# Kernel tuning notes

Hardware: AMD Instinct MI355X
Metric: run time of the kernel (lower is better)

Reference implementation:

```python
import jax, jax.numpy as jnp
import numpy as np

BN_EPS = 1e-5


def gcn_conv(x, src, dst, n, W, b):
    # PyG GCNConv: h = x @ W; add self-loops; symmetric deg^{-1/2} norm; scatter-add; + bias
    h = x @ W
    sl = jnp.arange(n, dtype=src.dtype)
    src_f = jnp.concatenate([src, sl])
    dst_f = jnp.concatenate([dst, sl])
    deg = jax.ops.segment_sum(jnp.ones_like(dst_f, dtype=h.dtype), dst_f, num_segments=n)
    dis = jnp.where(deg > 0, jax.lax.rsqrt(jnp.maximum(deg, 1.0)), 0.0)
    norm = dis[src_f] * dis[dst_f]                       # [E+N]
    msg = h[src_f] * norm[:, None]                       # gather + scale
    out = jax.ops.segment_sum(msg, dst_f, num_segments=n)  # scatter-add
    return out + b


def batchnorm(x, g, b):
    # training-mode BatchNorm1d (batch statistics), deterministic
    mu = jnp.mean(x, axis=0)
    var = jnp.mean((x - mu) ** 2, axis=0)
    return g * (x - mu) * jax.lax.rsqrt(var + BN_EPS) + b


def setup_inputs() -> dict:
    key = jax.random.key(0)
    ks = jax.random.split(key, 12)
    N, E, F_IN, D, M, G = 40000, 640000, 128, 128, 256, 2000
    x = jax.random.normal(ks[0], (N, F_IN), dtype=jnp.float32)
    edge_index = jax.random.randint(ks[1], (2, E), 0, N, dtype=jnp.int64)
    batch = jnp.sort(jax.random.randint(ks[2], (N,), 0, G, dtype=jnp.int64))
    s = lambda fi: 1.0 / np.sqrt(fi)
    W1 = jax.random.normal(ks[3], (F_IN, D), dtype=jnp.float32) * s(F_IN)
    b1 = jnp.zeros((D,), jnp.float32)
    W2 = jax.random.normal(ks[4], (D, D), dtype=jnp.float32) * s(D)
    b2 = jnp.zeros((D,), jnp.float32)
    bn1_g = jnp.ones((D,), jnp.float32); bn1_b = jnp.zeros((D,), jnp.float32)
    bn2_g = jnp.ones((D,), jnp.float32); bn2_b = jnp.zeros((D,), jnp.float32)
    fc1_w = jax.random.normal(ks[5], (D, M), dtype=jnp.float32) * s(D)
    fc1_b = jnp.zeros((M,), jnp.float32)
    fc2_w = jax.random.normal(ks[6], (M, M), dtype=jnp.float32) * s(M)
    fc2_b = jnp.zeros((M,), jnp.float32)
    fc3_w = jax.random.normal(ks[7], (M, 1), dtype=jnp.float32) * s(M)
    fc3_b = jnp.zeros((1,), jnp.float32)
    return dict(x=x, edge_index=edge_index, batch=batch, num_graphs=G,
                W1=W1, b1=b1, W2=W2, b2=b2,
                bn1_g=bn1_g, bn1_b=bn1_b, bn2_g=bn2_g, bn2_b=bn2_b,
                fc1_w=fc1_w, fc1_b=fc1_b, fc2_w=fc2_w, fc2_b=fc2_b,
                fc3_w=fc3_w, fc3_b=fc3_b)


def reference(x, edge_index, batch, num_graphs, W1, b1, W2, b2,
              bn1_g, bn1_b, bn2_g, bn2_b,
              fc1_w, fc1_b, fc2_w, fc2_b, fc3_w, fc3_b):
    n = x.shape[0]
    src, dst = edge_index[0], edge_index[1]
    h = gcn_conv(x, src, dst, n, W1, b1)
    h = jax.nn.relu(batchnorm(h, bn1_g, bn1_b))
    h = gcn_conv(h, src, dst, n, W2, b2)
    h = jax.nn.relu(batchnorm(h, bn2_g, bn2_b))
    g = jax.ops.segment_sum(h, batch, num_segments=num_graphs)  # scatter_sum pooling [G, D]
    g = jax.nn.relu(g @ fc1_w + fc1_b)   # dropout is identity in eval
    g = jax.nn.relu(g @ fc2_w + fc2_b)
    return g @ fc3_w + fc3_b             # [G, 1]
```

## Files before the change

### kernel.cpp

```cpp
#include <hip/hip_runtime.h>
#include <hip/hip_fp16.h>

#define NN 40000
#define NE 640000
#define DF 128
#define NG 2000
#define NCH 157
#define FILLB 625
#define G1_BLKS 313
#define G2_BLKS 625

typedef unsigned int u32;
typedef __attribute__((ext_vector_type(8))) short short8;
typedef __attribute__((ext_vector_type(4))) float floatx4;

__device__ inline float2 bf2_to_f2(u32 u) {
    return make_float2(__uint_as_float(u << 16), __uint_as_float(u & 0xffff0000u));
}
__device__ inline u32 f_to_bf(float f) {
    u32 u = __float_as_uint(f);
    return (u + 0x7fffu + ((u >> 16) & 1u)) >> 16;
}
__device__ inline u32 pack_bf2(float a, float b) {
    return f_to_bf(a) | (f_to_bf(b) << 16);
}
__device__ inline float bf_to_f(short s) {
    return __uint_as_float(((u32)(unsigned short)s) << 16);
}
__device__ inline float colw_to_f(int cw) {
    return __half2float(__ushort_as_half((unsigned short)((u32)cw >> 16)));
}

template<bool BF16IN, bool FUSE_BN, bool WT_F32, bool TILE128>
__device__ __forceinline__ void gemm_core(const void* __restrict__ Xv, const void* __restrict__ wsrc,
                                          u32* __restrict__ outb, const float* __restrict__ slots,
                                          const float* __restrict__ gam, const float* __restrict__ bet, int bid) {
    __shared__ unsigned short uni[128 * 136];
    __shared__ float sc[128], sh[128];
    unsigned short* wlds = uni;
    unsigned short* clds = uni;
    int tid = threadIdx.x;
    int row0 = bid * (TILE128 ? 128 : 64);

    if (FUSE_BN) {
        if (tid < 128) {
            float s = 0.f, q = 0.f;
            for (int k = 0; k < 64; k++) {
                s += slots[k * 256 + tid];
                q += slots[k * 256 + 128 + tid];
            }
            const float inv_n = 1.0f / (float)NN;
            float mu = s * inv_n;
            float va = fmaf(-mu, mu, q * inv_n);
            float a = gam[tid] * rsqrtf(va + 1e-5f);
            sc[tid] = a;
            sh[tid] = fmaf(-mu, a, bet[tid]);
        }
    }
    if (WT_F32) {
        const float* W = (const float*)wsrc;
        for (int i = tid; i < 16384; i += 256) {
            int k = i >> 7, c = i & 127;
            wlds[c * 136 + k] = (unsigned short)f_to_bf(W[i]);
        }
    } else {
        const unsigned short* wt = (const unsigned short*)wsrc;
        for (int i = tid; i < 2048; i += 256) {
            int c = i >> 4, s = i & 15;
            *(uint4*)&wlds[c * 136 + s * 8] = ((const uint4*)wt)[i];
        }
    }
    __syncthreads();

    int lane = tid & 63;
    int wave = tid >> 6;
    int qr = lane >> 4;
    int rl = lane & 15;

    if (TILE128) {
        int rA0 = row0 + wave * 32 + rl;
        int rA1 = rA0 + 16;
        int rA0c = rA0 < NN ? rA0 : NN - 1;
        int rA1c = rA1 < NN ? rA1 : NN - 1;
        floatx4 acc[2][8];
#pragma unroll
        for (int a = 0; a < 2; a++)
#pragma unroll
            for (int b = 0; b < 8; b++) acc[a][b] = (floatx4){0.f, 0.f, 0.f, 0.f};
#pragma unroll
        for (int kb = 0; kb < 4; kb++) {
            int k0 = kb * 32 + qr * 8;
            short8 a0, a1;
            if (!BF16IN) {
                const float* p0 = (const float*)Xv + (size_t)rA0c * DF + k0;
                const float* p1 = (const float*)Xv + (size_t)rA1c * DF + k0;
                float4 u0 = *(const float4*)p0, u1 = *(const float4*)(p0 + 4);
                float4 v0 = *(const float4*)p1, v1 = *(const float4*)(p1 + 4);
                float fa[8] = {u0.x, u0.y, u0.z, u0.w, u1.x, u1.y, u1.z, u1.w};
                float fb[8] = {v0.x, v0.y, v0.z, v0.w, v1.x, v1.y, v1.z, v1.w};
#pragma unroll
                for (int j = 0; j < 8; j++) { a0[j] = (short)f_to_bf(fa[j]); a1[j] = (short)f_to_bf(fb[j]); }
            } else {
                a0 = *(const short8*)((const u32*)Xv + (size_t)rA0c * 64 + (k0 >> 1));
                a1 = *(const short8*)((const u32*)Xv + (size_t)rA1c * 64 + (k0 >> 1));
                if (FUSE_BN) {
#pragma unroll
                    for (int j = 0; j < 8; j++) {
                        float f0 = fmaxf(fmaf(bf_to_f(a0[j]), sc[k0 + j], sh[k0 + j]), 0.f);
                        float f1 = fmaxf(fmaf(bf_to_f(a1[j]), sc[k0 + j], sh[k0 + j]), 0.f);
                        a0[j] = (short)f_to_bf(f0);
                        a1[j] = (short)f_to_bf(f1);
                    }
                }
            }
#pragma unroll
            for (int ct = 0; ct < 8; ct++) {
                short8 bfr = *(const short8*)&wlds[(ct * 16 + rl) * 136 + k0];
                acc[0][ct] = __builtin_amdgcn_mfma_f32_16x16x32_bf16(a0, bfr, acc[0][ct], 0, 0, 0);
                acc[1][ct] = __builtin_amdgcn_mfma_f32_16x16x32_bf16(a1, bfr, acc[1][ct], 0, 0, 0);
            }
        }
        __syncthreads();
#pragma unroll
        for (int rt = 0; rt < 2; rt++)
#pragma unroll
            for (int ct = 0; ct < 8; ct++)
#pragma unroll
                for (int r = 0; r < 4; r++) {
                    int lr = wave * 32 + rt * 16 + qr * 4 + r;
                    int c = ct * 16 + rl;
                    clds[lr * 136 + c] = (unsigned short)f_to_bf(acc[rt][ct][r]);
                }
        __syncthreads();
        for (int i = tid; i < 2048; i += 256) {
            int lr = i >> 4, s = i & 15;
            int grow = row0 + lr;
            if (grow < NN) {
                uint4 v = *(const uint4*)&clds[lr * 136 + s * 8];
                ((uint4*)(outb + (size_t)grow * 64))[s] = v;
            }
        }
    } else {
        int rA = row0 + wave * 16 + rl;
        floatx4 acc[8];
#pragma unroll
        for (int b = 0; b < 8; b++) acc[b] = (floatx4){0.f, 0.f, 0.f, 0.f};
#pragma unroll
        for (int kb = 0; kb < 4; kb++) {
            int k0 = kb * 32 + qr * 8;
            short8 a0;
            if (!BF16IN) {
                const float* p0 = (const float*)Xv + (size_t)rA * DF + k0;
                float4 u0 = *(const float4*)p0, u1 = *(const float4*)(p0 + 4);
                float fa[8] = {u0.x, u0.y, u0.z, u0.w, u1.x, u1.y, u1.z, u1.w};
#pragma unroll
                for (int j = 0; j < 8; j++) a0[j] = (short)f_to_bf(fa[j]);
            } else {
                a0 = *(const short8*)((const u32*)Xv + (size_t)rA * 64 + (k0 >> 1));
                if (FUSE_BN) {
#pragma unroll
                    for (int j = 0; j < 8; j++) {
                        float f0 = fmaxf(fmaf(bf_to_f(a0[j]), sc[k0 + j], sh[k0 + j]), 0.f);
                        a0[j] = (short)f_to_bf(f0);
                    }
                }
            }
#pragma unroll
            for (int ct = 0; ct < 8; ct++) {
                short8 bfr = *(const short8*)&wlds[(ct * 16 + rl) * 136 + k0];
                acc[ct] = __builtin_amdgcn_mfma_f32_16x16x32_bf16(a0, bfr, acc[ct], 0, 0, 0);
            }
        }
        __syncthreads();
#pragma unroll
        for (int ct = 0; ct < 8; ct++)
#pragma unroll
            for (int r = 0; r < 4; r++) {
                int lr = wave * 16 + qr * 4 + r;
                int c = ct * 16 + rl;
                clds[lr * 136 + c] = (unsigned short)f_to_bf(acc[ct][r]);
            }
        __syncthreads();
        for (int i = tid; i < 1024; i += 256) {
            int lr = i >> 4, s = i & 15;
            uint4 v = *(const uint4*)&clds[lr * 136 + s * 8];
            ((uint4*)(outb + (size_t)(row0 + lr) * 64))[s] = v;
        }
    }
}

__global__ __launch_bounds__(256, 4) void k_countgemm(const int* __restrict__ dst, int* __restrict__ deg,
                                                      int* __restrict__ rank,
                                                      const float* __restrict__ W1, const float* __restrict__ W2,
                                                      unsigned short* __restrict__ wt2,
                                                      const float* __restrict__ X, u32* __restrict__ outb) {
    int bid = blockIdx.x;
    if (bid < FILLB) {
        int e0 = bid * 1024 + threadIdx.x;
        int d0 = dst[e0], d1 = dst[e0 + 256], d2 = dst[e0 + 512], d3 = dst[e0 + 768];
        int r0 = atomicAdd(&deg[d0], 1);
        int r1 = atomicAdd(&deg[d1], 1);
        int r2 = atomicAdd(&deg[d2], 1);
        int r3 = atomicAdd(&deg[d3], 1);
        rank[e0] = r0;
        rank[e0 + 256] = r1;
        rank[e0 + 512] = r2;
        rank[e0 + 768] = r3;
        return;
    }
    if (bid == FILLB) {
        for (int i = threadIdx.x; i < 128 * 128; i += 256) {
            int k = i >> 7, c = i & 127;
            wt2[c * 128 + k] = (unsigned short)f_to_bf(W2[i]);
        }
        return;
    }
    gemm_core<false, false, true, true>(X, W1, outb, nullptr, nullptr, nullptr, bid - FILLB - 1);
}

__global__ __launch_bounds__(256) void k_scan(const int* __restrict__ deg,
                                              int* __restrict__ row_ptr, float* __restrict__ dis) {
    __shared__ int red[256];
    __shared__ int ls[256];
    int tid = threadIdx.x;
    int blk = blockIdx.x;
    int limit = blk * 256;
    int partial = 0;
    for (int i = tid; i < limit; i += 256) partial += deg[i];
    red[tid] = partial;
    int i = limit + tid;
    int d = (i < NN) ? deg[i] : 0;
    ls[tid] = d;
    __syncthreads();
#pragma unroll
    for (int off = 128; off > 0; off >>= 1) {
        if (tid < off) red[tid] += red[tid + off];
        __syncthreads();
    }
    int base = red[0];
#pragma unroll
    for (int off = 1; off < 256; off <<= 1) {
        int t = (tid >= off) ? ls[tid - off] : 0;
        __syncthreads();
        ls[tid] += t;
        __syncthreads();
    }
    if (i < NN) {
        int r = base + ls[tid] - d;
        row_ptr[i] = r;
        dis[i] = rsqrtf((float)(d + 1));
    }
    if (blk == NCH - 1 && tid == 0) row_ptr[NN] = NE;
}

__global__ __launch_bounds__(256) void k_fill(const int* __restrict__ src, const int* __restrict__ dst,
                                              const int* __restrict__ rank, const int* __restrict__ row_ptr,
                                              const float* __restrict__ dis, u32* __restrict__ col) {
    int e0 = blockIdx.x * 1024 + threadIdx.x;
    int d0 = dst[e0], d1 = dst[e0 + 256], d2 = dst[e0 + 512], d3 = dst[e0 + 768];
    int s0 = src[e0], s1 = src[e0 + 256], s2 = src[e0 + 512], s3 = src[e0 + 768];
    int r0 = rank[e0], r1 = rank[e0 + 256], r2 = rank[e0 + 512], r3 = rank[e0 + 768];
    u32 h0 = (u32)__half_as_ushort(__float2half(dis[s0]));
    u32 h1 = (u32)__half_as_ushort(__float2half(dis[s1]));
    u32 h2 = (u32)__half_as_ushort(__float2half(dis[s2]));
    u32 h3 = (u32)__half_as_ushort(__float2half(dis[s3]));
    col[row_ptr[d0] + r0] = (u32)s0 | (h0 << 16);
    col[row_ptr[d1] + r1] = (u32)s1 | (h1 << 16);
    col[row_ptr[d2] + r2] = (u32)s2 | (h2 << 16);
    col[row_ptr[d3] + r3] = (u32)s3 | (h3 << 16);
}

__global__ __launch_bounds__(256, 4) void k_gemm2(const u32* __restrict__ Hb, const unsigned short* __restrict__ wt2,
                                                  u32* __restrict__ outb, const float* __restrict__ slots,
                                                  const float* __restrict__ gam, const float* __restrict__ bet) {
    gemm_core<true, true, false, false>(Hb, wt2, outb, slots, gam, bet, blockIdx.x);
}

__global__ __launch_bounds__(256) void k_gather(const u32* __restrict__ Hb, const int* __restrict__ row_ptr,
                                                const u32* __restrict__ col, const float* __restrict__ dis,
                                                const float* __restrict__ bias, u32* __restrict__ outb,
                                                float* __restrict__ slots) {
    __shared__ float sred[4][128];
    __shared__ float qred[4][128];
    int t = threadIdx.x & 63;
    int wv = threadIdx.x >> 6;
    int node = blockIdx.x * 4 + wv;
    float di = dis[node];
    float2 acc;
    {
        float2 a = bf2_to_f2(Hb[(size_t)node * 64 + t]);
        float s = di * di;
        acc = make_float2(a.x * s, a.y * s);
    }
    int lo = row_ptr[node], hi = row_ptr[node + 1];
    for (int base = lo; base < hi; base += 64) {
        int m = hi - base; if (m > 64) m = 64;
        int cw = 0;
        if (t < m) cw = (int)col[base + t];
        int j = 0;
        for (; j + 8 <= m; j += 8) {
            int c0 = __shfl(cw, j),     c1 = __shfl(cw, j + 1);
            int c2 = __shfl(cw, j + 2), c3 = __shfl(cw, j + 3);
            int c4 = __shfl(cw, j + 4), c5 = __shfl(cw, j + 5);
            int c6 = __shfl(cw, j + 6), c7 = __shfl(cw, j + 7);
            u32 u0 = Hb[(size_t)(c0 & 0xffff) * 64 + t], u1 = Hb[(size_t)(c1 & 0xffff) * 64 + t];
            u32 u2 = Hb[(size_t)(c2 & 0xffff) * 64 + t], u3 = Hb[(size_t)(c3 & 0xffff) * 64 + t];
            u32 u4 = Hb[(size_t)(c4 & 0xffff) * 64 + t], u5 = Hb[(size_t)(c5 & 0xffff) * 64 + t];
            u32 u6 = Hb[(size_t)(c6 & 0xffff) * 64 + t], u7 = Hb[(size_t)(c7 & 0xffff) * 64 + t];
            float w0 = di * colw_to_f(c0), w1 = di * colw_to_f(c1);
            float w2 = di * colw_to_f(c2), w3 = di * colw_to_f(c3);
            float w4 = di * colw_to_f(c4), w5 = di * colw_to_f(c5);
            float w6 = di * colw_to_f(c6), w7 = di * colw_to_f(c7);
            float2 h0 = bf2_to_f2(u0), h1 = bf2_to_f2(u1), h2 = bf2_to_f2(u2), h3 = bf2_to_f2(u3);
            float2 h4 = bf2_to_f2(u4), h5 = bf2_to_f2(u5), h6 = bf2_to_f2(u6), h7 = bf2_to_f2(u7);
            acc.x = fmaf(h3.x, w3, fmaf(h2.x, w2, fmaf(h1.x, w1, fmaf(h0.x, w0, acc.x))));
            acc.y = fmaf(h3.y, w3, fmaf(h2.y, w2, fmaf(h1.y, w1, fmaf(h0.y, w0, acc.y))));
            acc.x = fmaf(h7.x, w7, fmaf(h6.x, w6, fmaf(h5.x, w5, fmaf(h4.x, w4, acc.x))));
            acc.y = fmaf(h7.y, w7, fmaf(h6.y, w6, fmaf(h5.y, w5, fmaf(h4.y, w4, acc.y))));
        }
        for (; j < m; j++) {
            int c0 = __shfl(cw, j);
            float w0 = di * colw_to_f(c0);
            float2 h0 = bf2_to_f2(Hb[(size_t)(c0 & 0xffff) * 64 + t]);
            acc.x = fmaf(h0.x, w0, acc.x);
            acc.y = fmaf(h0.y, w0, acc.y);
        }
    }
    float2 b = ((const float2*)bias)[t];
    acc.x += b.x; acc.y += b.y;
    outb[(size_t)node * 64 + t] = pack_bf2(acc.x, acc.y);
    sred[wv][2 * t] = acc.x;     sred[wv][2 * t + 1] = acc.y;
    qred[wv][2 * t] = acc.x * acc.x; qred[wv][2 * t + 1] = acc.y * acc.y;
    __syncthreads();
    int tid = threadIdx.x;
    if (tid < 128) {
        float s = sred[0][tid] + sred[1][tid] + sred[2][tid] + sred[3][tid];
        float q = qred[0][tid] + qred[1][tid] + qred[2][tid] + qred[3][tid];
        int slot = blockIdx.x & 63;
        atomicAdd(&slots[slot * 256 + tid], s);
        atomicAdd(&slots[slot * 256 + 128 + tid], q);
    }
}

__global__ __launch_bounds__(256) void k_poolfc(const u32* __restrict__ Hb, const int* __restrict__ batch,
                                                const float* __restrict__ slots,
                                                const float* __restrict__ gam, const float* __restrict__ bet,
                                                const float* __restrict__ fc1w, const float* __restrict__ fc1b,
                                                const float* __restrict__ fc2w, const float* __restrict__ fc2b,
                                                const float* __restrict__ fc3w, const float* __restrict__ fc3b,
                                                float* __restrict__ out) {
    __shared__ float sc[128], sh[128];
    __shared__ float pooled[4][128];
    __shared__ float g1[4][256];
    __shared__ float g2[4][256];
    __shared__ int bnds[5];
    int tid = threadIdx.x;
    int gbase = blockIdx.x * 4;
    if (tid < 128) {
        float s = 0.f, q = 0.f;
        for (int k = 0; k < 64; k++) {
            s += slots[k * 256 + tid];
            q += slots[k * 256 + 128 + tid];
        }
        const float inv_n = 1.0f / (float)NN;
        float mu = s * inv_n;
        float va = fmaf(-mu, mu, q * inv_n);
        float a = gam[tid] * rsqrtf(va + 1e-5f);
        sc[tid] = a;
        sh[tid] = fmaf(-mu, a, bet[tid]);
    } else if (tid < 133) {
        int target = gbase + (tid - 128);
        int a = 0, b = NN;
        while (a < b) { int m = (a + b) >> 1; if (batch[m] < target) a = m + 1; else b = m; }
        bnds[tid - 128] = a;
    }
    __syncthreads();
    {
        int g = tid >> 6, p = tid & 63;
        int lo = bnds[g], hi = bnds[g + 1];
        float a0 = 0.f, a1 = 0.f;
        float sc0 = sc[2 * p], sh0 = sh[2 * p], sc1 = sc[2 * p + 1], sh1 = sh[2 * p + 1];
        for (int i = lo; i < hi; i++) {
            float2 v = bf2_to_f2(Hb[(size_t)i * 64 + p]);
            a0 += fmaxf(fmaf(v.x, sc0, sh0), 0.f);
            a1 += fmaxf(fmaf(v.y, sc1, sh1), 0.f);
        }
        pooled[g][2 * p] = a0;
        pooled[g][2 * p + 1] = a1;
    }
    __syncthreads();
    {
        float x0 = 0.f, x1 = 0.f, x2 = 0.f, x3 = 0.f;
        for (int k = 0; k < 128; k++) {
            float wv = fc1w[k * 256 + tid];
            x0 = fmaf(pooled[0][k], wv, x0);
            x1 = fmaf(pooled[1][k], wv, x1);
            x2 = fmaf(pooled[2][k], wv, x2);
            x3 = fmaf(pooled[3][k], wv, x3);
        }
        float bb = fc1b[tid];
        g1[0][tid] = fmaxf(x0 + bb, 0.f);
        g1[1][tid] = fmaxf(x1 + bb, 0.f);
        g1[2][tid] = fmaxf(x2 + bb, 0.f);
        g1[3][tid] = fmaxf(x3 + bb, 0.f);
    }
    __syncthreads();
    {
        float x0 = 0.f, x1 = 0.f, x2 = 0.f, x3 = 0.f;
        for (int k = 0; k < 256; k++) {
            float wv = fc2w[k * 256 + tid];
            x0 = fmaf(g1[0][k], wv, x0);
            x1 = fmaf(g1[1][k], wv, x1);
            x2 = fmaf(g1[2][k], wv, x2);
            x3 = fmaf(g1[3][k], wv, x3);
        }
        float bb = fc2b[tid];
        g2[0][tid] = fmaxf(x0 + bb, 0.f);
        g2[1][tid] = fmaxf(x1 + bb, 0.f);
        g2[2][tid] = fmaxf(x2 + bb, 0.f);
        g2[3][tid] = fmaxf(x3 + bb, 0.f);
    }
    __syncthreads();
    {
        int lane = tid & 63, wv = tid >> 6;
        float s = fmaf(g2[wv][lane], fc3w[lane],
                  fmaf(g2[wv][64 + lane], fc3w[64 + lane],
                  fmaf(g2[wv][128 + lane], fc3w[128 + lane],
                       g2[wv][192 + lane] * fc3w[192 + lane])));
        for (int off = 32; off > 0; off >>= 1) s += __shfl_down(s, off);
        if (lane == 0) out[gbase + wv] = s + fc3b[0];
    }
}

extern "C" void kernel_launch(void* const* d_in, const int* in_sizes, int n_in,
                              void* d_out, int out_size, void* d_ws, size_t ws_size,
                              hipStream_t stream) {
    const float* x    = (const float*)d_in[0];
    const int*   ei   = (const int*)d_in[1];
    const int*   batch= (const int*)d_in[2];
    const float* W1   = (const float*)d_in[4];
    const float* b1   = (const float*)d_in[5];
    const float* W2   = (const float*)d_in[6];
    const float* b2   = (const float*)d_in[7];
    const float* bn1g = (const float*)d_in[8];
    const float* bn1b = (const float*)d_in[9];
    const float* bn2g = (const float*)d_in[10];
    const float* bn2b = (const float*)d_in[11];
    const float* fc1w = (const float*)d_in[12];
    const float* fc1b = (const float*)d_in[13];
    const float* fc2w = (const float*)d_in[14];
    const float* fc2b = (const float*)d_in[15];
    const float* fc3w = (const float*)d_in[16];
    const float* fc3b = (const float*)d_in[17];
    const int* src = ei;
    const int* dst = ei + NE;
    float* outp = (float*)d_out;

    char* w = (char*)d_ws;
    size_t o = 0;
    auto alloc = [&](size_t bytes) -> char* {
        char* p = w + o;
        o = (o + bytes + 255) & ~(size_t)255;
        return p;
    };
    int*   deg     = (int*)alloc((size_t)NN * 4);
    float* slotsA  = (float*)alloc(64 * 256 * 4);
    float* slotsB  = (float*)alloc(64 * 256 * 4);
    char*  zend    = w + o;
    int*   row_ptr = (int*)alloc((size_t)(NN + 1) * 4);
    int*   rank    = (int*)alloc((size_t)NE * 4);
    u32*   col     = (u32*)alloc((size_t)NE * 4);
    float* dis     = (float*)alloc((size_t)NN * 4);
    unsigned short* wt2 = (unsigned short*)alloc(128 * 128 * 2);
    u32*   bufA    = (u32*)alloc((size_t)NN * 64 * 4);
    u32*   bufB    = (u32*)alloc((size_t)NN * 64 * 4);

    hipMemsetAsync(deg, 0, (size_t)(zend - (char*)deg), stream);

    k_countgemm<<<FILLB + 1 + G1_BLKS, 256, 0, stream>>>(dst, deg, rank, W1, W2, wt2, x, bufA);
    k_scan<<<NCH, 256, 0, stream>>>(deg, row_ptr, dis);
    k_fill<<<FILLB, 256, 0, stream>>>(src, dst, rank, row_ptr, dis, col);
    k_gather<<<NN / 4, 256, 0, stream>>>(bufA, row_ptr, col, dis, b1, bufB, slotsA);
    k_gemm2<<<G2_BLKS, 256, 0, stream>>>(bufB, wt2, bufA, slotsA, bn1g, bn1b);
    k_gather<<<NN / 4, 256, 0, stream>>>(bufA, row_ptr, col, dis, b2, bufB, slotsB);
    k_poolfc<<<NG / 4, 256, 0, stream>>>(bufB, batch, slotsB, bn2g, bn2b,
                                         fc1w, fc1b, fc2w, fc2b, fc3w, fc3b, outp);
}
```

Before: 272.8 us.

## Replace global atomic degree counting with chunked LDS histograms and two-level scan

Degree counting moves from global atomicAdd per edge to per-block shared-memory histograms: 64 edge chunks by 8 node octants, written as a chunk-major degree table. The scan kernel now also builds per-chunk base offsets, and fill adds them to compute CSR positions. Slot buffers are zeroed inside the first kernel, which removes the separate memset. The cost is that each histogram block reads its entire edge chunk (an 8x redundant dst read) and that 64xNPAD degree and base tables are written and read. CSR order within a row also becomes deterministic.

Measured after the change: 260.5 us. -4.5%, faster.

```diff
diff --git a/kernel.cpp b/kernel.cpp
--- a/kernel.cpp
+++ b/kernel.cpp
@@ -9,6 +9,13 @@
 #define FILLB 625
 #define G1_BLKS 313
 #define G2_BLKS 625
+#define NCHUNK 64
+#define ECH 10000
+#define NOCT 8
+#define QN 5120
+#define NPAD (NOCT * QN)
+#define NWIN 160
+#define HISTB (NCHUNK * NOCT)
 
 typedef unsigned int u32;
 typedef __attribute__((ext_vector_type(8))) short short8;
@@ -34,11 +41,10 @@
 template<bool BF16IN, bool FUSE_BN, bool WT_F32, bool TILE128>
 __device__ __forceinline__ void gemm_core(const void* __restrict__ Xv, const void* __restrict__ wsrc,
                                           u32* __restrict__ outb, const float* __restrict__ slots,
-                                          const float* __restrict__ gam, const float* __restrict__ bet, int bid) {
-    __shared__ unsigned short uni[128 * 136];
-    __shared__ float sc[128], sh[128];
-    unsigned short* wlds = uni;
-    unsigned short* clds = uni;
+                                          const float* __restrict__ gam, const float* __restrict__ bet,
+                                          int bid, char* sbuf, float* sc, float* sh) {
+    unsigned short* wlds = (unsigned short*)sbuf;
+    unsigned short* clds = (unsigned short*)sbuf;
     int tid = threadIdx.x;
     int row0 = bid * (TILE128 ? 128 : 64);
 
@@ -189,47 +195,77 @@
     }
 }
 
-__global__ __launch_bounds__(256, 4) void k_countgemm(const int* __restrict__ dst, int* __restrict__ deg,
-                                                      int* __restrict__ rank,
+__global__ __launch_bounds__(256, 4) void k_countgemm(const int* __restrict__ dst,
+                                                      int* __restrict__ degT, int* __restrict__ rank,
+                                                      int* __restrict__ wsum, float* __restrict__ slots0,
                                                       const float* __restrict__ W1, const float* __restrict__ W2,
                                                       unsigned short* __restrict__ wt2,
                                                       const float* __restrict__ X, u32* __restrict__ outb) {
+    __shared__ __align__(16) char sbuf[34816];
+    __shared__ float sc[128], sh[128];
     int bid = blockIdx.x;
-    if (bid < FILLB) {
-        int e0 = bid * 1024 + threadIdx.x;
-        int d0 = dst[e0], d1 = dst[e0 + 256], d2 = dst[e0 + 512], d3 = dst[e0 + 768];
-        int r0 = atomicAdd(&deg[d0], 1);
-        int r1 = atomicAdd(&deg[d1], 1);
-        int r2 = atomicAdd(&deg[d2], 1);
-        int r3 = atomicAdd(&deg[d3], 1);
-        rank[e0] = r0;
-        rank[e0 + 256] = r1;
-        rank[e0 + 512] = r2;
-        rank[e0 + 768] = r3;
+    int tid = threadIdx.x;
+    if (bid < HISTB) {
+        int c = bid >> 3, oct = bid & 7;
+        int nlo = oct * QN;
+        int* hist = (int*)sbuf;
+        for (int i = tid; i < QN; i += 256) hist[i] = 0;
+        __syncthreads();
+        int ebase = c * ECH;
+        for (int i = tid; i < ECH; i += 256) {
+            int d = dst[ebase + i];
+            int t = d - nlo;
+            if ((u32)t < (u32)QN) rank[ebase + i] = atomicAdd(&hist[t], 1);
+        }
+        __syncthreads();
+        for (int i = tid; i < QN; i += 256) degT[(size_t)c * NPAD + nlo + i] = hist[i];
+        int wv = tid >> 6, lane = tid & 63;
+        for (int lw = wv; lw < 20; lw += 4) {
+            int v = hist[lw * 256 + lane] + hist[lw * 256 + 64 + lane]
+                  + hist[lw * 256 + 128 + lane] + hist[lw * 256 + 192 + lane];
+            for (int off = 32; off > 0; off >>= 1) v += __shfl_down(v, off);
+            if (lane == 0) wsum[c * NWIN + oct * 20 + lw] = v;
+        }
         return;
     }
-    if (bid == FILLB) {
-        for (int i = threadIdx.x; i < 128 * 128; i += 256) {
-            int k = i >> 7, c = i & 127;
-            wt2[c * 128 + k] = (unsigned short)f_to_bf(W2[i]);
-        }
+    if (bid < HISTB + 2) {
+        float* s = slots0 + (size_t)(bid - HISTB) * 64 * 256;
+        for (int i = tid; i < 64 * 256; i += 256) s[i] = 0.f;
         return;
     }
-    gemm_core<false, false, true, true>(X, W1, outb, nullptr, nullptr, nullptr, bid - FILLB - 1);
-}
-
-__global__ __launch_bounds__(256) void k_scan(const int* __restrict__ deg,
+    if (bid == HISTB + 2) {
+        for (int i = tid; i < 128 * 128; i += 256) {
+            int k = i >> 7, cc = i & 127;
+            wt2[cc * 128 + k] = (unsigned short)f_to_bf(W2[i]);
+        }
+        return;
+    }
+    gemm_core<false, false, true, true>(X, W1, outb, nullptr, nullptr, nullptr,
+                                        bid - HISTB - 3, sbuf, sc, sh);
+}
+
+__global__ __launch_bounds__(256) void k_scan(const int* __restrict__ degT, const int* __restrict__ wsum,
+                                              int* __restrict__ baseT,
                                               int* __restrict__ row_ptr, float* __restrict__ dis) {
     __shared__ int red[256];
     __shared__ int ls[256];
     int tid = threadIdx.x;
-    int blk = blockIdx.x;
-    int limit = blk * 256;
-    int partial = 0;
-    for (int i = tid; i < limit; i += 256) partial += deg[i];
-    red[tid] = partial;
-    int i = limit + tid;
-    int d = (i < NN) ? deg[i] : 0;
+    int wnd = blockIdx.x;
+    int part = 0;
+    for (int idx = tid; idx < NCHUNK * NWIN; idx += 256) {
+        int wp = idx % NWIN;
+        if (wp < wnd) part += wsum[idx];
+    }
+    red[tid] = part;
+    int n = wnd * 256 + tid;
+    int run = 0;
+#pragma unroll 4
+    for (int c = 0; c < NCHUNK; c++) {
+        int v = degT[(size_t)c * NPAD + n];
+        baseT[(size_t)c * NPAD + n] = run;
+        run += v;
+    }
+    int d = run;
     ls[tid] = d;
     __syncthreads();
 #pragma unroll
@@ -245,35 +281,37 @@
         ls[tid] += t;
         __syncthreads();
     }
-    if (i < NN) {
+    if (n < NN) {
         int r = base + ls[tid] - d;
-        row_ptr[i] = r;
-        dis[i] = rsqrtf((float)(d + 1));
-    }
-    if (blk == NCH - 1 && tid == 0) row_ptr[NN] = NE;
+        row_ptr[n] = r;
+        dis[n] = rsqrtf((float)(d + 1));
+    }
+    if (wnd == NCH - 1 && tid == 0) row_ptr[NN] = NE;
 }
 
 __global__ __launch_bounds__(256) void k_fill(const int* __restrict__ src, const int* __restrict__ dst,
                                               const int* __restrict__ rank, const int* __restrict__ row_ptr,
+                                              const int* __restrict__ baseT,
                                               const float* __restrict__ dis, u32* __restrict__ col) {
     int e0 = blockIdx.x * 1024 + threadIdx.x;
-    int d0 = dst[e0], d1 = dst[e0 + 256], d2 = dst[e0 + 512], d3 = dst[e0 + 768];
-    int s0 = src[e0], s1 = src[e0 + 256], s2 = src[e0 + 512], s3 = src[e0 + 768];
-    int r0 = rank[e0], r1 = rank[e0 + 256], r2 = rank[e0 + 512], r3 = rank[e0 + 768];
-    u32 h0 = (u32)__half_as_ushort(__float2half(dis[s0]));
-    u32 h1 = (u32)__half_as_ushort(__float2half(dis[s1]));
-    u32 h2 = (u32)__half_as_ushort(__float2half(dis[s2]));
-    u32 h3 = (u32)__half_as_ushort(__float2half(dis[s3]));
-    col[row_ptr[d0] + r0] = (u32)s0 | (h0 << 16);
-    col[row_ptr[d1] + r1] = (u32)s1 | (h1 << 16);
-    col[row_ptr[d2] + r2] = (u32)s2 | (h2 << 16);
-    col[row_ptr[d3] + r3] = (u32)s3 | (h3 << 16);
+#pragma unroll
+    for (int q = 0; q < 4; q++) {
+        int e = e0 + q * 256;
+        int d = dst[e];
+        int s = src[e];
+        int r = rank[e];
+        int c = e / ECH;
+        u32 h = (u32)__half_as_ushort(__float2half(dis[s]));
+        col[row_ptr[d] + baseT[(size_t)c * NPAD + d] + r] = (u32)s | (h << 16);
+    }
 }
 
 __global__ __launch_bounds__(256, 4) void k_gemm2(const u32* __restrict__ Hb, const unsigned short* __restrict__ wt2,
                                                   u32* __restrict__ outb, const float* __restrict__ slots,
                                                   const float* __restrict__ gam, const float* __restrict__ bet) {
-    gemm_core<true, true, false, false>(Hb, wt2, outb, slots, gam, bet, blockIdx.x);
+    __shared__ __align__(16) char sbuf[34816];
+    __shared__ float sc[128], sh[128];
+    gemm_core<true, true, false, false>(Hb, wt2, outb, slots, gam, bet, blockIdx.x, sbuf, sc, sh);
 }
 
 __global__ __launch_bounds__(256) void k_gather(const u32* __restrict__ Hb, const int* __restrict__ row_ptr,
@@ -463,10 +501,10 @@
         o = (o + bytes + 255) & ~(size_t)255;
         return p;
     };
-    int*   deg     = (int*)alloc((size_t)NN * 4);
-    float* slotsA  = (float*)alloc(64 * 256 * 4);
-    float* slotsB  = (float*)alloc(64 * 256 * 4);
-    char*  zend    = w + o;
+    int*   degT    = (int*)alloc((size_t)NCHUNK * NPAD * 4);
+    int*   baseT   = (int*)alloc((size_t)NCHUNK * NPAD * 4);
+    int*   wsum    = (int*)alloc((size_t)NCHUNK * NWIN * 4);
+    float* slots0  = (float*)alloc((size_t)2 * 64 * 256 * 4);
     int*   row_ptr = (int*)alloc((size_t)(NN + 1) * 4);
     int*   rank    = (int*)alloc((size_t)NE * 4);
     u32*   col     = (u32*)alloc((size_t)NE * 4);
@@ -474,12 +512,13 @@
     unsigned short* wt2 = (unsigned short*)alloc(128 * 128 * 2);
     u32*   bufA    = (u32*)alloc((size_t)NN * 64 * 4);
     u32*   bufB    = (u32*)alloc((size_t)NN * 64 * 4);
-
-    hipMemsetAsync(deg, 0, (size_t)(zend - (char*)deg), stream);
-
-    k_countgemm<<<FILLB + 1 + G1_BLKS, 256, 0, stream>>>(dst, deg, rank, W1, W2, wt2, x, bufA);
-    k_scan<<<NCH, 256, 0, stream>>>(deg, row_ptr, dis);
-    k_fill<<<FILLB, 256, 0, stream>>>(src, dst, rank, row_ptr, dis, col);
+    float* slotsA  = slots0;
+    float* slotsB  = slots0 + 64 * 256;
+
+    k_countgemm<<<HISTB + 3 + G1_BLKS, 256, 0, stream>>>(dst, degT, rank, wsum, slots0,
+                                                         W1, W2, wt2, x, bufA);
+    k_scan<<<NCH, 256, 0, stream>>>(degT, wsum, baseT, row_ptr, dis);
+    k_fill<<<FILLB, 256, 0, stream>>>(src, dst, rank, row_ptr, baseT, dis, col);
     k_gather<<<NN / 4, 256, 0, stream>>>(bufA, row_ptr, col, dis, b1, bufB, slotsA);
     k_gemm2<<<G2_BLKS, 256, 0, stream>>>(bufB, wt2, bufA, slotsA, bn1g, bn1b);
     k_gather<<<NN / 4, 256, 0, stream>>>(bufA, row_ptr, col, dis, b2, bufB, slotsB);
```
